# Kernel optimization log

Hardware: AMD Instinct MI355X
Metric: run time of the kernel (lower is better)

Reference implementation:

```python
import jax, jax.numpy as jnp
import numpy as np

N_EMBD = 1024
N_HEAD = 16
HEAD_SIZE = N_EMBD // N_HEAD
B, T = 2, 2048
LN_EPS = 1e-5


def _layernorm(x, g, b):
    mu = jnp.mean(x, axis=-1, keepdims=True)
    var = jnp.var(x, axis=-1, keepdims=True)
    return (x - mu) * jax.lax.rsqrt(var + LN_EPS) * g + b


def setup_inputs() -> dict:
    key = jax.random.key(0)
    ks = jax.random.split(key, 12)
    s_in = 1.0 / np.sqrt(N_EMBD)
    s_ff = 1.0 / np.sqrt(4 * N_EMBD)
    return {
        "x": jax.random.normal(ks[0], (B, T, N_EMBD), jnp.float32),
        # per-head q/k/v linears stacked head-major: [n_embd, n_embd]
        "Wq": jax.random.uniform(ks[1], (N_EMBD, N_EMBD), jnp.float32, -s_in, s_in),
        "Wk": jax.random.uniform(ks[2], (N_EMBD, N_EMBD), jnp.float32, -s_in, s_in),
        "Wv": jax.random.uniform(ks[3], (N_EMBD, N_EMBD), jnp.float32, -s_in, s_in),
        "Wo": jax.random.uniform(ks[4], (N_EMBD, N_EMBD), jnp.float32, -s_in, s_in),
        "bo": jax.random.uniform(ks[5], (N_EMBD,), jnp.float32, -s_in, s_in),
        "W1": jax.random.uniform(ks[6], (N_EMBD, 4 * N_EMBD), jnp.float32, -s_in, s_in),
        "b1": jax.random.uniform(ks[7], (4 * N_EMBD,), jnp.float32, -s_in, s_in),
        "W2": jax.random.uniform(ks[8], (4 * N_EMBD, N_EMBD), jnp.float32, -s_ff, s_ff),
        "b2": jax.random.uniform(ks[9], (N_EMBD,), jnp.float32, -s_ff, s_ff),
        "g1": jnp.ones((N_EMBD,), jnp.float32),
        "be1": jnp.zeros((N_EMBD,), jnp.float32),
        "g2": jnp.ones((N_EMBD,), jnp.float32),
        "be2": jnp.zeros((N_EMBD,), jnp.float32),
    }


def reference(x, Wq, Wk, Wv, Wo, bo, W1, b1, W2, b2, g1, be1, g2, be2):
    Bx, Tx, C = x.shape
    # --- self-attention on ln1(x) ---
    h = _layernorm(x, g1, be1)
    q = (h @ Wq).reshape(Bx, Tx, N_HEAD, HEAD_SIZE)
    k = (h @ Wk).reshape(Bx, Tx, N_HEAD, HEAD_SIZE)
    v = (h @ Wv).reshape(Bx, Tx, N_HEAD, HEAD_SIZE)
    # NOTE: faithful to source -- scale uses full C (n_embd), not head_size
    scale = C ** (-0.5)
    wei = jnp.einsum("bqhd,bkhd->bhqk", q, k) * scale  # [B,H,T,T]
    causal = jnp.tril(jnp.ones((Tx, Tx), bool))
    wei = jnp.where(causal, wei, -jnp.inf)
    wei = jax.nn.softmax(wei, axis=-1)
    attn = jnp.einsum("bhqk,bkhd->bqhd", wei, v).reshape(Bx, Tx, C)
    x = x + (attn @ Wo + bo)
    # --- feed-forward on ln2(x) ---
    h2 = _layernorm(x, g2, be2)
    x = x + (jax.nn.relu(h2 @ W1 + b1) @ W2 + b2)
    return x
```

## Files before the change

kernel.cpp:

```cpp
#include <hip/hip_runtime.h>
#include <hip/hip_bf16.h>
#include <math.h>

#define BB 2
#define TT 2048
#define CC 1024
#define NH 16
#define HD 64
#define BT (BB*TT)
#define LN_EPS 1e-5f
#define ATT_SCALE 0.03125f

typedef __bf16 bf16x8 __attribute__((ext_vector_type(8)));
typedef __bf16 bf16x4 __attribute__((ext_vector_type(4)));
typedef short shortx4 __attribute__((ext_vector_type(4)));
typedef float floatx4 __attribute__((ext_vector_type(4)));

__device__ __forceinline__ void gl_lds16(const __bf16* g, __bf16* l) {
    __builtin_amdgcn_global_load_lds((const __attribute__((address_space(1))) void*)g,
                                     (__attribute__((address_space(3))) void*)l,
                                     16, 0, 0);
}

#define MFMA32(a, b, c) __builtin_amdgcn_mfma_f32_16x16x32_bf16(a, b, c, 0, 0, 0)

#if __has_builtin(__builtin_amdgcn_mfma_f32_16x16x16_bf16)
__device__ __forceinline__ floatx4 mfma16(bf16x4 a, bf16x4 b, floatx4 c) {
    return __builtin_amdgcn_mfma_f32_16x16x16_bf16(a, b, c, 0, 0, 0);
}
#else
__device__ __forceinline__ floatx4 mfma16(bf16x4 a, bf16x4 b, floatx4 c) {
    return __builtin_amdgcn_mfma_f32_16x16x16bf16_1k(
        __builtin_bit_cast(shortx4, a), __builtin_bit_cast(shortx4, b), c, 0, 0, 0);
}
#endif

__device__ __forceinline__ void swizzle_xcd(int& xb, int& yb, int& zb) {
    int nx = gridDim.x, ny = gridDim.y;
    int total = nx * ny * (int)gridDim.z;
    int lin = blockIdx.x + nx * (blockIdx.y + ny * blockIdx.z);
    int c = lin & 7, s = lin >> 3;
    int idx = c * (total >> 3) + s;
    xb = idx % nx;
    yb = (idx / nx) % ny;
    zb = idx / (nx * ny);
}

__global__ __launch_bounds__(256) void transpose_ln(
        const float* __restrict__ Wq, const float* __restrict__ Wk,
        const float* __restrict__ Wv, const float* __restrict__ Wo,
        const float* __restrict__ W1, const float* __restrict__ W2,
        __bf16* __restrict__ WqkvT, __bf16* __restrict__ WoT,
        __bf16* __restrict__ W1T, __bf16* __restrict__ W2T,
        const float* __restrict__ x, const float* __restrict__ g1,
        const float* __restrict__ be1, __bf16* __restrict__ hb) {
    __shared__ float t[32][33];
    __shared__ float rs_[4], rss_[4];
    __shared__ float mu_s, inv_s;
    int idx = blockIdx.x;
    if (idx >= 12288) {
        int row = idx - 12288;
        const float4* xr = (const float4*)(x + (size_t)row * CC);
        float4 v = xr[threadIdx.x];
        float s  = v.x + v.y + v.z + v.w;
        float ss = v.x*v.x + v.y*v.y + v.z*v.z + v.w*v.w;
        #pragma unroll
        for (int off = 32; off; off >>= 1) {
            s  += __shfl_down(s, off);
            ss += __shfl_down(ss, off);
        }
        int lane = threadIdx.x & 63, wid = threadIdx.x >> 6;
        if (lane == 0) { rs_[wid] = s; rss_[wid] = ss; }
        __syncthreads();
        if (threadIdx.x == 0) {
            float S  = rs_[0] + rs_[1] + rs_[2] + rs_[3];
            float SS = rss_[0] + rss_[1] + rss_[2] + rss_[3];
            float mu  = S * (1.0f / CC);
            float var = SS * (1.0f / CC) - mu * mu;
            mu_s  = mu;
            inv_s = rsqrtf(var + LN_EPS);
        }
        __syncthreads();
        float mu = mu_s, inv = inv_s;
        float4 gv = ((const float4*)g1)[threadIdx.x];
        float4 bv = ((const float4*)be1)[threadIdx.x];
        bf16x4 o;
        o[0] = (__bf16)((v.x - mu) * inv * gv.x + bv.x);
        o[1] = (__bf16)((v.y - mu) * inv * gv.y + bv.y);
        o[2] = (__bf16)((v.z - mu) * inv * gv.z + bv.z);
        o[3] = (__bf16)((v.w - mu) * inv * gv.w + bv.w);
        *(bf16x4*)(hb + (size_t)row * CC + threadIdx.x * 4) = o;
        return;
    }
    const float* src; __bf16* dst; int K, N, tn, tk;
    if (idx < 3072) {
        int wsel = idx >> 10, local = idx & 1023;
        src = (wsel == 0) ? Wq : (wsel == 1 ? Wk : Wv);
        dst = WqkvT + (size_t)wsel * 1024 * 1024;
        K = 1024; N = 1024; tn = local & 31; tk = local >> 5;
    } else if (idx < 4096) {
        int local = idx - 3072;
        src = Wo; dst = WoT; K = 1024; N = 1024; tn = local & 31; tk = local >> 5;
    } else if (idx < 8192) {
        int local = idx - 4096;
        src = W1; dst = W1T; K = 1024; N = 4096; tn = local & 127; tk = local >> 7;
    } else {
        int local = idx - 8192;
        src = W2; dst = W2T; K = 4096; N = 1024; tn = local & 31; tk = local >> 5;
    }
    int n0 = tn * 32, k0 = tk * 32;
    int tx = threadIdx.x & 31, ty = threadIdx.x >> 5;
    #pragma unroll
    for (int r = ty; r < 32; r += 8)
        t[r][tx] = src[(size_t)(k0 + r) * N + n0 + tx];
    __syncthreads();
    #pragma unroll
    for (int r = ty; r < 32; r += 8)
        dst[(size_t)(n0 + r) * K + k0 + tx] = (__bf16)t[tx][r];
}

__global__ __launch_bounds__(256) void reduce_wo_ln(const __bf16* __restrict__ P,
                                                    const float* __restrict__ bo,
                                                    const float* __restrict__ x,
                                                    const float* __restrict__ g2,
                                                    const float* __restrict__ be2,
                                                    float* __restrict__ x2,
                                                    __bf16* __restrict__ hb) {
    int row = blockIdx.x;
    int c = threadIdx.x * 4;
    bf16x4 a0 = *(const bf16x4*)(P + (size_t)row * CC + c);
    bf16x4 a1 = *(const bf16x4*)(P + (size_t)BT * CC + (size_t)row * CC + c);
    float4 xb = *(const float4*)(x + (size_t)row * CC + c);
    float4 bb = *(const float4*)(bo + c);
    float4 v;
    v.x = xb.x + bb.x + (float)a0[0] + (float)a1[0];
    v.y = xb.y + bb.y + (float)a0[1] + (float)a1[1];
    v.z = xb.z + bb.z + (float)a0[2] + (float)a1[2];
    v.w = xb.w + bb.w + (float)a0[3] + (float)a1[3];
    *(float4*)(x2 + (size_t)row * CC + c) = v;

    float s  = v.x + v.y + v.z + v.w;
    float ss = v.x*v.x + v.y*v.y + v.z*v.z + v.w*v.w;
    #pragma unroll
    for (int off = 32; off; off >>= 1) {
        s  += __shfl_down(s, off);
        ss += __shfl_down(ss, off);
    }
    __shared__ float rs_[4], rss_[4];
    __shared__ float mu_s, inv_s;
    int lane = threadIdx.x & 63, wid = threadIdx.x >> 6;
    if (lane == 0) { rs_[wid] = s; rss_[wid] = ss; }
    __syncthreads();
    if (threadIdx.x == 0) {
        float S  = rs_[0] + rs_[1] + rs_[2] + rs_[3];
        float SS = rss_[0] + rss_[1] + rss_[2] + rss_[3];
        float mu  = S * (1.0f / CC);
        float var = SS * (1.0f / CC) - mu * mu;
        mu_s  = mu;
        inv_s = rsqrtf(var + LN_EPS);
    }
    __syncthreads();
    float mu = mu_s, inv = inv_s;
    float4 gv = ((const float4*)g2)[threadIdx.x];
    float4 bv = ((const float4*)be2)[threadIdx.x];
    bf16x4 o;
    o[0] = (__bf16)((v.x - mu) * inv * gv.x + bv.x);
    o[1] = (__bf16)((v.y - mu) * inv * gv.y + bv.y);
    o[2] = (__bf16)((v.z - mu) * inv * gv.z + bv.z);
    o[3] = (__bf16)((v.w - mu) * inv * gv.w + bv.w);
    *(bf16x4*)(hb + (size_t)row * CC + c) = o;
}

__global__ __launch_bounds__(256) void reduce_ffn(const __bf16* __restrict__ P,
                                                  const float* __restrict__ b2,
                                                  const float* __restrict__ x2,
                                                  float* __restrict__ out) {
    int row = blockIdx.x;
    int c = threadIdx.x * 4;
    const size_t S = (size_t)BT * CC;
    float4 v = *(const float4*)(x2 + (size_t)row * CC + c);
    float4 bb = *(const float4*)(b2 + c);
    v.x += bb.x; v.y += bb.y; v.z += bb.z; v.w += bb.w;
    #pragma unroll
    for (int z = 0; z < 4; ++z) {
        bf16x4 a = *(const bf16x4*)(P + z * S + (size_t)row * CC + c);
        v.x += (float)a[0]; v.y += (float)a[1]; v.z += (float)a[2]; v.w += (float)a[3];
    }
    *(float4*)(out + (size_t)row * CC + c) = v;
}

template<int NT, int SK, typename OT, bool BIAS, bool RELU, bool RES, bool VSPLIT>
__global__ __launch_bounds__(256) void gemm_bf16(const __bf16* __restrict__ A,
                                                 const __bf16* __restrict__ Bt,
                                                 const float* __restrict__ bias,
                                                 const float* __restrict__ res,
                                                 OT* __restrict__ C,
                                                 __bf16* __restrict__ vt,
                                                 int M, int N, int K) {
    constexpr int JN = NT / 32;
    __shared__ __bf16 As[128 * 64];
    __shared__ __bf16 Bs[NT * 64];
    int bx, by, bz;
    swizzle_xcd(bx, by, bz);
    const int tid = threadIdx.x;
    const int l = tid & 63, w = tid >> 6;
    const int m = l & 15, g = l >> 4;
    const int wm = w >> 1, wn = w & 1;
    const int m0 = by * 128, n0 = bx * NT;
    const int Keff = K / SK;
    const int kbase = (SK > 1) ? bz * Keff : 0;

    const int srow = l >> 3;
    const int sko  = ((l & 7) ^ ((l >> 3) & 7)) * 8;

    floatx4 acc[4][JN];
    #pragma unroll
    for (int i = 0; i < 4; ++i)
        #pragma unroll
        for (int j = 0; j < JN; ++j) {
            floatx4 z = {0.f, 0.f, 0.f, 0.f};
            acc[i][j] = z;
        }

    for (int kt = 0; kt < Keff; kt += 64) {
        __syncthreads();
        #pragma unroll
        for (int c = 0; c < 4; ++c) {
            int idx = w * 4 + c;
            gl_lds16(A + (size_t)(m0 + idx * 8 + srow) * K + kbase + kt + sko,
                     As + idx * 512);
        }
        #pragma unroll
        for (int c = 0; c < JN; ++c) {
            int idx = w * JN + c;
            gl_lds16(Bt + (size_t)(n0 + idx * 8 + srow) * K + kbase + kt + sko,
                     Bs + idx * 512);
        }
        __syncthreads();

        #pragma unroll
        for (int hf = 0; hf < 2; ++hf) {
            const int co = (((hf * 4 + g) ^ (m & 7)) * 8);
            bf16x8 af[4], bfr[JN];
            #pragma unroll
            for (int i = 0; i < 4; ++i)
                af[i] = *(const bf16x8*)&As[(wm * 64 + i * 16 + m) * 64 + co];
            #pragma unroll
            for (int j = 0; j < JN; ++j)
                bfr[j] = *(const bf16x8*)&Bs[(wn * (NT / 2) + j * 16 + m) * 64 + co];
            #pragma unroll
            for (int i = 0; i < 4; ++i)
                #pragma unroll
                for (int j = 0; j < JN; ++j)
                    acc[i][j] = MFMA32(af[i], bfr[j], acc[i][j]);
        }
    }

    if (SK > 1) {
        __bf16* P = (__bf16*)C + (size_t)bz * M * N;
        #pragma unroll
        for (int i = 0; i < 4; ++i) {
            int row = m0 + wm * 64 + i * 16 + g * 4;
            #pragma unroll
            for (int j = 0; j < JN; ++j) {
                int col = n0 + wn * (NT / 2) + j * 16 + m;
                #pragma unroll
                for (int r = 0; r < 4; ++r)
                    P[(size_t)(row + r) * N + col] = (__bf16)acc[i][j][r];
            }
        }
    } else if (VSPLIT && n0 >= 2048) {
        #pragma unroll
        for (int i = 0; i < 4; ++i) {
            int row = m0 + wm * 64 + i * 16 + g * 4;
            int bb = row >> 11, t0 = row & 2047;
            #pragma unroll
            for (int j = 0; j < JN; ++j) {
                int cv = n0 + wn * (NT / 2) + j * 16 + m - 2048;
                bf16x4 o;
                #pragma unroll
                for (int r = 0; r < 4; ++r) o[r] = (__bf16)acc[i][j][r];
                *(bf16x4*)(vt + ((size_t)(bb * NH + (cv >> 6)) * HD + (cv & 63)) * 2048 + t0) = o;
            }
        }
    } else {
        #pragma unroll
        for (int i = 0; i < 4; ++i) {
            int row = m0 + wm * 64 + i * 16 + g * 4;
            #pragma unroll
            for (int j = 0; j < JN; ++j) {
                int col = n0 + wn * (NT / 2) + j * 16 + m;
                float bv = BIAS ? bias[col] : 0.0f;
                #pragma unroll
                for (int r = 0; r < 4; ++r) {
                    float vo = acc[i][j][r] + bv;
                    if (RELU) vo = fmaxf(vo, 0.0f);
                    if (RES)  vo += res[(size_t)(row + r) * N + col];
                    C[(size_t)(row + r) * N + col] = (OT)vo;
                }
            }
        }
    }
}

__global__ __launch_bounds__(256, 2) void attn_mfma3(const __bf16* __restrict__ qkv,
                                                     const __bf16* __restrict__ vt,
                                                     __bf16* __restrict__ att) {
    const int lin = blockIdx.x;
    const int half = lin >> 8, pid = lin & 255;
    const int q0 = pid & 7, h = (pid >> 3) & 15, b = pid >> 7;
    const int qt = half ? 15 - q0 : q0;

    const int tid = threadIdx.x;
    const int l = tid & 63, w = tid >> 6;
    const int m = l & 15, g = l >> 4;

    __shared__ __bf16 Ks[2][128][32];
    __shared__ __bf16 Vt3[8][64][16];

    const __bf16* qp = qkv + (size_t)b * TT * 3072 + h * HD;
    const __bf16* kp = qp + 1024;
    const __bf16* vh = vt + (size_t)(b * NH + h) * HD * 2048;

    bf16x8 qb[2][2];
    #pragma unroll
    for (int nt = 0; nt < 2; ++nt) {
        int qrow = qt * 128 + w * 32 + nt * 16 + m;
        qb[nt][0] = *(const bf16x8*)(qp + (size_t)qrow * 3072 + g * 8);
        qb[nt][1] = *(const bf16x8*)(qp + (size_t)qrow * 3072 + 32 + g * 8);
    }

    floatx4 O[2][4];
    float l_s[2] = {0.0f, 0.0f};
    #pragma unroll
    for (int nt = 0; nt < 2; ++nt)
        #pragma unroll
        for (int jd = 0; jd < 4; ++jd) {
            floatx4 z = {0.f, 0.f, 0.f, 0.f};
            O[nt][jd] = z;
        }

    for (int kt = 0; kt <= qt; ++kt) {
        __syncthreads();
        #pragma unroll
        for (int c = 0; c < 4; ++c) {
            int idx = w * 4 + c;
            int dh = idx >> 3, k16 = idx & 7;
            gl_lds16(kp + (size_t)(kt * 128 + k16 * 16 + (l >> 2)) * 3072
                        + dh * 32 + (((l & 3) ^ ((l >> 3) & 3)) * 8),
                     (__bf16*)Ks + dh * 4096 + k16 * 512);
        }
        #pragma unroll
        for (int c = 0; c < 4; ++c) {
            int idx = w * 4 + c;
            int jt = idx >> 1, dhf = idx & 1;
            gl_lds16(vh + (size_t)(dhf * 32 + (l >> 1)) * 2048 + kt * 128
                        + jt * 16 + (((l & 1) ^ ((l >> 3) & 1)) * 8),
                     (__bf16*)Vt3 + jt * 1024 + dhf * 512);
        }
        __syncthreads();

        floatx4 S[2][8];
        #pragma unroll
        for (int jt = 0; jt < 8; ++jt) {
            int co = (g ^ ((m >> 1) & 3)) * 8;
            bf16x8 kf0 = *(const bf16x8*)&Ks[0][jt * 16 + m][co];
            bf16x8 kf1 = *(const bf16x8*)&Ks[1][jt * 16 + m][co];
            #pragma unroll
            for (int nt = 0; nt < 2; ++nt) {
                floatx4 z = {0.f, 0.f, 0.f, 0.f};
                z = MFMA32(kf0, qb[nt][0], z);
                S[nt][jt] = MFMA32(kf1, qb[nt][1], z);
            }
        }

        bf16x4 pv[2][8];
        const bool last = (kt == qt);
        #pragma unroll
        for (int nt = 0; nt < 2; ++nt) {
            if (last) {
                int qr = w * 32 + nt * 16 + m;
                #pragma unroll
                for (int jt = 0; jt < 8; ++jt)
                    #pragma unroll
                    for (int r = 0; r < 4; ++r)
                        if (jt * 16 + g * 4 + r > qr) S[nt][jt][r] = -1e30f;
            }
            float ls = 0.0f;
            #pragma unroll
            for (int jt = 0; jt < 8; ++jt) {
                bf16x4 t;
                #pragma unroll
                for (int r = 0; r < 4; ++r) {
                    float p = __expf(S[nt][jt][r] * ATT_SCALE);
                    ls += p;
                    t[r] = (__bf16)p;
                }
                pv[nt][jt] = t;
            }
            l_s[nt] += ls;
        }

        #pragma unroll
        for (int jt = 0; jt < 8; ++jt)
            #pragma unroll
            for (int jd = 0; jd < 4; ++jd) {
                bf16x4 vf = *(const bf16x4*)&Vt3[jt][jd * 16 + m]
                                [((g >> 1) ^ ((m >> 2) & 1)) * 8 + (g & 1) * 4];
                #pragma unroll
                for (int nt = 0; nt < 2; ++nt)
                    O[nt][jd] = mfma16(vf, pv[nt][jt], O[nt][jd]);
            }
    }

    #pragma unroll
    for (int nt = 0; nt < 2; ++nt) {
        float lsum = l_s[nt];
        lsum += __shfl_xor(lsum, 16, 64);
        lsum += __shfl_xor(lsum, 32, 64);
        float inv = 1.0f / lsum;
        int qrow = qt * 128 + w * 32 + nt * 16 + m;
        #pragma unroll
        for (int jd = 0; jd < 4; ++jd) {
            bf16x4 o;
            #pragma unroll
            for (int r = 0; r < 4; ++r) o[r] = (__bf16)(O[nt][jd][r] * inv);
            *(bf16x4*)(att + ((size_t)b * TT + qrow) * CC + h * HD + jd * 16 + g * 4) = o;
        }
    }
}

extern "C" void kernel_launch(void* const* d_in, const int* in_sizes, int n_in,
                              void* d_out, int out_size, void* d_ws, size_t ws_size,
                              hipStream_t stream) {
    const float* x   = (const float*)d_in[0];
    const float* Wq  = (const float*)d_in[1];
    const float* Wk  = (const float*)d_in[2];
    const float* Wv  = (const float*)d_in[3];
    const float* Wo  = (const float*)d_in[4];
    const float* bo  = (const float*)d_in[5];
    const float* W1  = (const float*)d_in[6];
    const float* b1  = (const float*)d_in[7];
    const float* W2  = (const float*)d_in[8];
    const float* b2  = (const float*)d_in[9];
    const float* g1  = (const float*)d_in[10];
    const float* be1 = (const float*)d_in[11];
    const float* g2  = (const float*)d_in[12];
    const float* be2 = (const float*)d_in[13];
    float* out = (float*)d_out;

    char* p = (char*)d_ws;
    char*   pool  = p;          p += (size_t)32 * 1024 * 1024;
    __bf16* qkvb  = (__bf16*)pool;
    __bf16* vtb   = (__bf16*)(pool + (size_t)BT * 3072 * 2);
    __bf16* wop   = (__bf16*)pool;
    __bf16* ffp   = (__bf16*)pool;
    __bf16* attb  = (__bf16*)p; p += (size_t)BT * CC * 2;
    __bf16* hb    = (__bf16*)p; p += (size_t)BT * CC * 2;
    float*  x2    = (float*)p;  p += (size_t)BT * CC * 4;
    __bf16* ffb   = (__bf16*)p; p += (size_t)BT * 4096 * 2;
    __bf16* WqkvT = (__bf16*)p; p += (size_t)3072 * 1024 * 2;
    __bf16* WoT   = (__bf16*)p; p += (size_t)1024 * 1024 * 2;
    __bf16* W1T   = (__bf16*)p; p += (size_t)4096 * 1024 * 2;
    __bf16* W2T   = (__bf16*)p; p += (size_t)1024 * 4096 * 2;

    transpose_ln<<<16384, 256, 0, stream>>>(Wq, Wk, Wv, Wo, W1, W2,
                                            WqkvT, WoT, W1T, W2T,
                                            x, g1, be1, hb);
    gemm_bf16<128, 1, __bf16, false, false, false, true><<<dim3(24, 32), 256, 0, stream>>>(
        hb, WqkvT, nullptr, nullptr, qkvb, vtb, BT, 3072, 1024);
    attn_mfma3<<<512, 256, 0, stream>>>(qkvb, vtb, attb);
    gemm_bf16<64, 2, __bf16, false, false, false, false><<<dim3(16, 32, 2), 256, 0, stream>>>(
        attb, WoT, nullptr, nullptr, wop, nullptr, BT, 1024, 1024);
    reduce_wo_ln<<<BT, 256, 0, stream>>>(wop, bo, x, g2, be2, x2, hb);
    gemm_bf16<128, 1, __bf16, true, true, false, false><<<dim3(32, 32), 256, 0, stream>>>(
        hb, W1T, b1, nullptr, ffb, nullptr, BT, 4096, 1024);
    gemm_bf16<128, 4, __bf16, false, false, false, false><<<dim3(8, 32, 4), 256, 0, stream>>>(
        ffb, W2T, nullptr, nullptr, ffp, nullptr, BT, 1024, 4096);
    reduce_ffn<<<BT, 256, 0, stream>>>(ffp, b2, x2, out);
}
```

Baseline: 339.1 us.

## Replace GEMMs with 256x256 tile, 8-wave, double-buffered pipelined bf16 GEMM

```diff
diff --git a/kernel.cpp b/kernel.cpp
--- a/kernel.cpp
+++ b/kernel.cpp
@@ -34,6 +34,12 @@
         __builtin_bit_cast(shortx4, a), __builtin_bit_cast(shortx4, b), c, 0, 0, 0);
 }
 #endif
+
+#define BARRIER() __builtin_amdgcn_s_barrier()
+#define MEMF()  asm volatile("" ::: "memory")
+#define LGKM0() asm volatile("s_waitcnt lgkmcnt(0)" ::: "memory")
+#define VM4()   asm volatile("s_waitcnt vmcnt(4)" ::: "memory")
+#define VM0()   asm volatile("s_waitcnt vmcnt(0)" ::: "memory")
 
 __device__ __forceinline__ void swizzle_xcd(int& xb, int& yb, int& zb) {
     int nx = gridDim.x, ny = gridDim.y;
@@ -189,117 +195,180 @@
     *(float4*)(out + (size_t)row * CC + c) = v;
 }
 
-template<int NT, int SK, typename OT, bool BIAS, bool RELU, bool RES, bool VSPLIT>
-__global__ __launch_bounds__(256) void gemm_bf16(const __bf16* __restrict__ A,
-                                                 const __bf16* __restrict__ Bt,
-                                                 const float* __restrict__ bias,
-                                                 const float* __restrict__ res,
-                                                 OT* __restrict__ C,
-                                                 __bf16* __restrict__ vt,
-                                                 int M, int N, int K) {
-    constexpr int JN = NT / 32;
-    __shared__ __bf16 As[128 * 64];
-    __shared__ __bf16 Bs[NT * 64];
+struct Frags { bf16x8 a[4][2]; bf16x8 b[2][2]; };
+
+__device__ __forceinline__ void stage_half(const __bf16* __restrict__ mat, int row0,
+                                           int ldk, int k0, __bf16* lds, int tid) {
+    int r = tid >> 3;
+    int lch = (tid & 7) ^ (r & 7);
+    const __bf16* gp = mat + (size_t)(row0 + r) * ldk + k0 + lch * 8;
+    gl_lds16(gp, lds + tid * 8);
+    gl_lds16(gp + (size_t)64 * ldk, lds + 4096 + tid * 8);
+}
+
+template<int QR, int QC>
+__device__ __forceinline__ void phase_loads(const __bf16* As_, const __bf16* Bs_,
+                                            int wr, int wc, int m, int g, Frags& f) {
+    #pragma unroll
+    for (int i = 0; i < 4; ++i) {
+        int ra = QR * 128 + wr * 64 + i * 16 + m;
+        #pragma unroll
+        for (int kk = 0; kk < 2; ++kk)
+            f.a[i][kk] = *(const bf16x8*)&As_[ra * 64 + (((kk * 4 + g) ^ (m & 7)) * 8)];
+    }
+    #pragma unroll
+    for (int j = 0; j < 2; ++j) {
+        int rb = QC * 128 + wc * 32 + j * 16 + m;
+        #pragma unroll
+        for (int kk = 0; kk < 2; ++kk)
+            f.b[j][kk] = *(const bf16x8*)&Bs_[rb * 64 + (((kk * 4 + g) ^ (m & 7)) * 8)];
+    }
+}
+
+template<int QR, int QC>
+__device__ __forceinline__ void phase_mfma(Frags& f, floatx4 (&acc)[2][2][4][2]) {
+    __builtin_amdgcn_s_setprio(1);
+    #pragma unroll
+    for (int i = 0; i < 4; ++i)
+        #pragma unroll
+        for (int j = 0; j < 2; ++j)
+            #pragma unroll
+            for (int kk = 0; kk < 2; ++kk)
+                acc[QR][QC][i][j] = MFMA32(f.a[i][kk], f.b[j][kk], acc[QR][QC][i][j]);
+    __builtin_amdgcn_s_setprio(0);
+}
+
+template<int SK, typename OT, bool BIAS, bool RELU, bool VSPLIT>
+__global__ __launch_bounds__(512, 2) void gemm256(const __bf16* __restrict__ A,
+                                                  const __bf16* __restrict__ Bt,
+                                                  const float* __restrict__ bias,
+                                                  OT* __restrict__ C,
+                                                  __bf16* __restrict__ vt,
+                                                  int M, int N, int K) {
+    __shared__ __bf16 As[2][16384];
+    __shared__ __bf16 Bs[2][16384];
     int bx, by, bz;
     swizzle_xcd(bx, by, bz);
     const int tid = threadIdx.x;
     const int l = tid & 63, w = tid >> 6;
     const int m = l & 15, g = l >> 4;
-    const int wm = w >> 1, wn = w & 1;
-    const int m0 = by * 128, n0 = bx * NT;
+    const int wr = w >> 2, wc = w & 3;
+    const int m0 = by * 256, n0 = bx * 256;
     const int Keff = K / SK;
-    const int kbase = (SK > 1) ? bz * Keff : 0;
-
-    const int srow = l >> 3;
-    const int sko  = ((l & 7) ^ ((l >> 3) & 7)) * 8;
-
-    floatx4 acc[4][JN];
-    #pragma unroll
-    for (int i = 0; i < 4; ++i)
-        #pragma unroll
-        for (int j = 0; j < JN; ++j) {
-            floatx4 z = {0.f, 0.f, 0.f, 0.f};
-            acc[i][j] = z;
-        }
-
-    for (int kt = 0; kt < Keff; kt += 64) {
-        __syncthreads();
-        #pragma unroll
-        for (int c = 0; c < 4; ++c) {
-            int idx = w * 4 + c;
-            gl_lds16(A + (size_t)(m0 + idx * 8 + srow) * K + kbase + kt + sko,
-                     As + idx * 512);
-        }
-        #pragma unroll
-        for (int c = 0; c < JN; ++c) {
-            int idx = w * JN + c;
-            gl_lds16(Bt + (size_t)(n0 + idx * 8 + srow) * K + kbase + kt + sko,
-                     Bs + idx * 512);
-        }
-        __syncthreads();
-
-        #pragma unroll
-        for (int hf = 0; hf < 2; ++hf) {
-            const int co = (((hf * 4 + g) ^ (m & 7)) * 8);
-            bf16x8 af[4], bfr[JN];
+    const int kb = (SK > 1) ? bz * Keff : 0;
+    const int iters = Keff >> 7;
+
+    floatx4 acc[2][2][4][2];
+    #pragma unroll
+    for (int a = 0; a < 2; ++a)
+        #pragma unroll
+        for (int b = 0; b < 2; ++b)
             #pragma unroll
             for (int i = 0; i < 4; ++i)
-                af[i] = *(const bf16x8*)&As[(wm * 64 + i * 16 + m) * 64 + co];
-            #pragma unroll
-            for (int j = 0; j < JN; ++j)
-                bfr[j] = *(const bf16x8*)&Bs[(wn * (NT / 2) + j * 16 + m) * 64 + co];
-            #pragma unroll
-            for (int i = 0; i < 4; ++i)
-                #pragma unroll
-                for (int j = 0; j < JN; ++j)
-                    acc[i][j] = MFMA32(af[i], bfr[j], acc[i][j]);
-        }
+                #pragma unroll
+                for (int j = 0; j < 2; ++j) {
+                    floatx4 z = {0.f, 0.f, 0.f, 0.f};
+                    acc[a][b][i][j] = z;
+                }
+
+    stage_half(A,  m0,       K, kb,      &As[0][0],    tid);
+    stage_half(Bt, n0,       K, kb,      &Bs[0][0],    tid);
+    stage_half(Bt, n0 + 128, K, kb,      &Bs[0][8192], tid);
+    stage_half(A,  m0 + 128, K, kb,      &As[0][8192], tid);
+    stage_half(A,  m0,       K, kb + 64, &As[1][0],    tid);
+    stage_half(Bt, n0 + 128, K, kb + 64, &Bs[1][8192], tid);
+    VM4(); BARRIER(); MEMF();
+
+    for (int it = 0; it < iters; ++it) {
+        const bool lastI = (it == iters - 1);
+        const int kB = kb + (2 * it + 1) * 64;
+        const int kC = kB + 64;
+        const int kD = kC + 64;
+
+        { Frags f; phase_loads<0,0>(&As[0][0], &Bs[0][0], wr, wc, m, g, f);
+          stage_half(Bt, n0, K, kB, &Bs[1][0], tid);
+          BARRIER(); LGKM0(); phase_mfma<0,0>(f, acc); BARRIER(); MEMF(); }
+        { Frags f; phase_loads<0,1>(&As[0][0], &Bs[0][0], wr, wc, m, g, f);
+          stage_half(A, m0 + 128, K, kB, &As[1][8192], tid);
+          BARRIER(); LGKM0(); phase_mfma<0,1>(f, acc); BARRIER(); MEMF(); }
+        { Frags f; phase_loads<1,1>(&As[0][0], &Bs[0][0], wr, wc, m, g, f);
+          if (!lastI) stage_half(A, m0, K, kC, &As[0][0], tid);
+          BARRIER(); LGKM0(); phase_mfma<1,1>(f, acc); BARRIER(); MEMF(); }
+        { Frags f; phase_loads<1,0>(&As[0][0], &Bs[0][0], wr, wc, m, g, f);
+          if (!lastI) { stage_half(Bt, n0 + 128, K, kC, &Bs[0][8192], tid);
+                        VM4(); }
+          else VM0();
+          BARRIER(); LGKM0(); phase_mfma<1,0>(f, acc); BARRIER(); MEMF(); }
+        { Frags f; phase_loads<0,0>(&As[1][0], &Bs[1][0], wr, wc, m, g, f);
+          if (!lastI) stage_half(Bt, n0, K, kC, &Bs[0][0], tid);
+          BARRIER(); LGKM0(); phase_mfma<0,0>(f, acc); BARRIER(); MEMF(); }
+        { Frags f; phase_loads<0,1>(&As[1][0], &Bs[1][0], wr, wc, m, g, f);
+          if (!lastI) stage_half(A, m0 + 128, K, kC, &As[0][8192], tid);
+          BARRIER(); LGKM0(); phase_mfma<0,1>(f, acc); BARRIER(); MEMF(); }
+        { Frags f; phase_loads<1,1>(&As[1][0], &Bs[1][0], wr, wc, m, g, f);
+          if (!lastI) stage_half(A, m0, K, kD, &As[1][0], tid);
+          BARRIER(); LGKM0(); phase_mfma<1,1>(f, acc); BARRIER(); MEMF(); }
+        { Frags f; phase_loads<1,0>(&As[1][0], &Bs[1][0], wr, wc, m, g, f);
+          if (!lastI) { stage_half(Bt, n0 + 128, K, kD, &Bs[1][8192], tid);
+                        VM4(); }
+          BARRIER(); LGKM0(); phase_mfma<1,0>(f, acc); BARRIER(); MEMF(); }
     }
 
     if (SK > 1) {
         __bf16* P = (__bf16*)C + (size_t)bz * M * N;
         #pragma unroll
-        for (int i = 0; i < 4; ++i) {
-            int row = m0 + wm * 64 + i * 16 + g * 4;
-            #pragma unroll
-            for (int j = 0; j < JN; ++j) {
-                int col = n0 + wn * (NT / 2) + j * 16 + m;
-                #pragma unroll
-                for (int r = 0; r < 4; ++r)
-                    P[(size_t)(row + r) * N + col] = (__bf16)acc[i][j][r];
-            }
-        }
+        for (int qr = 0; qr < 2; ++qr)
+            #pragma unroll
+            for (int i = 0; i < 4; ++i) {
+                int row = m0 + qr * 128 + wr * 64 + i * 16 + g * 4;
+                #pragma unroll
+                for (int qc = 0; qc < 2; ++qc)
+                    #pragma unroll
+                    for (int j = 0; j < 2; ++j) {
+                        int col = n0 + qc * 128 + wc * 32 + j * 16 + m;
+                        #pragma unroll
+                        for (int r = 0; r < 4; ++r)
+                            P[(size_t)(row + r) * N + col] = (__bf16)acc[qr][qc][i][j][r];
+                    }
+            }
     } else if (VSPLIT && n0 >= 2048) {
         #pragma unroll
-        for (int i = 0; i < 4; ++i) {
-            int row = m0 + wm * 64 + i * 16 + g * 4;
-            int bb = row >> 11, t0 = row & 2047;
-            #pragma unroll
-            for (int j = 0; j < JN; ++j) {
-                int cv = n0 + wn * (NT / 2) + j * 16 + m - 2048;
-                bf16x4 o;
-                #pragma unroll
-                for (int r = 0; r < 4; ++r) o[r] = (__bf16)acc[i][j][r];
-                *(bf16x4*)(vt + ((size_t)(bb * NH + (cv >> 6)) * HD + (cv & 63)) * 2048 + t0) = o;
-            }
-        }
+        for (int qr = 0; qr < 2; ++qr)
+            #pragma unroll
+            for (int i = 0; i < 4; ++i) {
+                int row = m0 + qr * 128 + wr * 64 + i * 16 + g * 4;
+                int bb = row >> 11, t0 = row & 2047;
+                #pragma unroll
+                for (int qc = 0; qc < 2; ++qc)
+                    #pragma unroll
+                    for (int j = 0; j < 2; ++j) {
+                        int cv = n0 + qc * 128 + wc * 32 + j * 16 + m - 2048;
+                        bf16x4 o;
+                        #pragma unroll
+                        for (int r = 0; r < 4; ++r) o[r] = (__bf16)acc[qr][qc][i][j][r];
+                        *(bf16x4*)(vt + ((size_t)(bb * NH + (cv >> 6)) * HD + (cv & 63)) * 2048 + t0) = o;
+                    }
+            }
     } else {
         #pragma unroll
-        for (int i = 0; i < 4; ++i) {
-            int row = m0 + wm * 64 + i * 16 + g * 4;
-            #pragma unroll
-            for (int j = 0; j < JN; ++j) {
-                int col = n0 + wn * (NT / 2) + j * 16 + m;
-                float bv = BIAS ? bias[col] : 0.0f;
-                #pragma unroll
-                for (int r = 0; r < 4; ++r) {
-                    float vo = acc[i][j][r] + bv;
-                    if (RELU) vo = fmaxf(vo, 0.0f);
-                    if (RES)  vo += res[(size_t)(row + r) * N + col];
-                    C[(size_t)(row + r) * N + col] = (OT)vo;
-                }
-            }
-        }
+        for (int qr = 0; qr < 2; ++qr)
+            #pragma unroll
+            for (int i = 0; i < 4; ++i) {
+                int row = m0 + qr * 128 + wr * 64 + i * 16 + g * 4;
+                #pragma unroll
+                for (int qc = 0; qc < 2; ++qc)
+                    #pragma unroll
+                    for (int j = 0; j < 2; ++j) {
+                        int col = n0 + qc * 128 + wc * 32 + j * 16 + m;
+                        float bv = BIAS ? bias[col] : 0.0f;
+                        #pragma unroll
+                        for (int r = 0; r < 4; ++r) {
+                            float vo = acc[qr][qc][i][j][r] + bv;
+                            if (RELU) vo = fmaxf(vo, 0.0f);
+                            C[(size_t)(row + r) * N + col] = (OT)vo;
+                        }
+                    }
+            }
     }
 }
 
@@ -467,15 +536,15 @@
     transpose_ln<<<16384, 256, 0, stream>>>(Wq, Wk, Wv, Wo, W1, W2,
                                             WqkvT, WoT, W1T, W2T,
                                             x, g1, be1, hb);
-    gemm_bf16<128, 1, __bf16, false, false, false, true><<<dim3(24, 32), 256, 0, stream>>>(
-        hb, WqkvT, nullptr, nullptr, qkvb, vtb, BT, 3072, 1024);
+    gemm256<1, __bf16, false, false, true><<<dim3(12, 16), 512, 0, stream>>>(
+        hb, WqkvT, nullptr, qkvb, vtb, BT, 3072, 1024);
     attn_mfma3<<<512, 256, 0, stream>>>(qkvb, vtb, attb);
-    gemm_bf16<64, 2, __bf16, false, false, false, false><<<dim3(16, 32, 2), 256, 0, stream>>>(
-        attb, WoT, nullptr, nullptr, wop, nullptr, BT, 1024, 1024);
+    gemm256<2, __bf16, false, false, false><<<dim3(4, 16, 2), 512, 0, stream>>>(
+        attb, WoT, nullptr, wop, nullptr, BT, 1024, 1024);
     reduce_wo_ln<<<BT, 256, 0, stream>>>(wop, bo, x, g2, be2, x2, hb);
-    gemm_bf16<128, 1, __bf16, true, true, false, false><<<dim3(32, 32), 256, 0, stream>>>(
-        hb, W1T, b1, nullptr, ffb, nullptr, BT, 4096, 1024);
-    gemm_bf16<128, 4, __bf16, false, false, false, false><<<dim3(8, 32, 4), 256, 0, stream>>>(
-        ffb, W2T, nullptr, nullptr, ffp, nullptr, BT, 1024, 4096);
+    gemm256<1, __bf16, true, true, false><<<dim3(16, 16), 512, 0, stream>>>(
+        hb, W1T, b1, ffb, nullptr, BT, 4096, 1024);
+    gemm256<4, __bf16, false, false, false><<<dim3(4, 16, 4), 512, 0, stream>>>(
+        ffb, W2T, nullptr, ffp, nullptr, BT, 1024, 4096);
     reduce_ffn<<<BT, 256, 0, stream>>>(ffp, b2, x2, out);
 }
```

Measured after the change: 356.0 us. 5.0% more time.
